# Performance work log

Hardware: AMD Instinct MI355X
Metric: run time of the kernel (lower is better)

## Reference

```python
import jax, jax.numpy as jnp
from jax import lax
import numpy as np

NUM_LABELS = 15
LABEL_TO_ID = {"O": 0, "B-PERSON": 1, "I-PERSON": 2, "B-LOCATION": 3, "I-LOCATION": 4,
               "B-ORGANIZATION": 5, "I-ORGANIZATION": 6, "B-PHONE": 7, "I-PHONE": 8,
               "B-EMAIL": 9, "I-EMAIL": 10, "B-ID_NUMBER": 11, "I-ID_NUMBER": 12,
               "B-ADDRESS": 13, "I-ADDRESS": 14}


def _pii_constraints():
    """Replicates EnhancedPIICRF._setup_transition_constraints."""
    forbidden = -10000.0
    c = np.zeros((NUM_LABELS, NUM_LABELS), dtype=np.float32)
    pii_types = ['PERSON', 'LOCATION', 'ORGANIZATION', 'PHONE', 'EMAIL', 'ID_NUMBER', 'ADDRESS']
    for t in pii_types:
        b_idx = LABEL_TO_ID[f'B-{t}']
        i_idx = LABEL_TO_ID[f'I-{t}']
        for o in pii_types:
            if o != t:
                c[LABEL_TO_ID[f'B-{o}'], i_idx] = forbidden
        if t in ['PHONE', 'EMAIL', 'ID_NUMBER']:
            c[i_idx, i_idx] = -1.0
    return jnp.asarray(c)


def setup_inputs() -> dict:
    key = jax.random.key(0)
    k1, k2, k3, k4, k5 = jax.random.split(key, 5)
    B, T, L = 512, 4096, NUM_LABELS
    emissions = jax.random.normal(k1, (B, T, L), dtype=jnp.float32)
    labels = jax.random.randint(k2, (B, T), 0, L, dtype=jnp.int64)
    mask = jnp.ones((B, T), dtype=jnp.bool_)
    # torchcrf init: uniform(-0.1, 0.1); constraints added to transitions
    transitions = jax.random.uniform(k3, (L, L), jnp.float32, -0.1, 0.1) + _pii_constraints()
    start_transitions = jax.random.uniform(k4, (L,), jnp.float32, -0.1, 0.1)
    end_transitions = jax.random.uniform(k5, (L,), jnp.float32, -0.1, 0.1)
    return {"emissions": emissions, "transitions": transitions,
            "start_transitions": start_transitions, "end_transitions": end_transitions,
            "labels": labels, "mask": mask}


def reference(emissions, transitions, start_transitions, end_transitions, labels, mask):
    """loss = -mean log-likelihood (torchcrf reduction='mean')."""
    B, T, L = emissions.shape
    maskf = mask.astype(emissions.dtype)
    labels = labels.astype(jnp.int32)

    # ---- numerator: score of the gold path (fully vectorized) ----
    em_score = jnp.take_along_axis(emissions, labels[..., None], axis=2)[..., 0]  # [B,T]
    em_score = (em_score * maskf).sum(axis=1)
    trans_score = (transitions[labels[:, :-1], labels[:, 1:]] * maskf[:, 1:]).sum(axis=1)
    seq_ends = mask.sum(axis=1).astype(jnp.int32) - 1
    last_tags = labels[jnp.arange(B), seq_ends]
    numerator = (start_transitions[labels[:, 0]] + em_score + trans_score
                 + end_transitions[last_tags])

    # ---- denominator: forward algorithm (log-sum-exp recurrence) ----
    alpha0 = start_transitions[None, :] + emissions[:, 0]  # [B,L]

    def step(alpha, xs):
        em_t, m_t = xs  # [B,L], [B]
        nxt = jax.nn.logsumexp(alpha[:, :, None] + transitions[None], axis=1) + em_t
        return jnp.where(m_t[:, None], nxt, alpha), None

    em_T = jnp.swapaxes(emissions, 0, 1)[1:]   # [T-1,B,L]
    mk_T = jnp.swapaxes(mask, 0, 1)[1:]        # [T-1,B]
    alpha, _ = lax.scan(step, alpha0, (em_T, mk_T))
    denominator = jax.nn.logsumexp(alpha + end_transitions[None, :], axis=1)

    llh = numerator - denominator
    return -jnp.mean(llh)
```

## Files before the change

### kernel.cpp

```cpp
#include <hip/hip_runtime.h>


typedef __attribute__((ext_vector_type(8))) __bf16 bf16x8;
typedef __attribute__((ext_vector_type(4))) float f32x4;
typedef __attribute__((ext_vector_type(2))) float f32x2;

#define BATCH 512
#define TLEN  4096
#define NCH   16
#define CLEN  256
#define LOG2E 1.44269504088896340736f
#define LN2   0.69314718055994530942f

__device__ __forceinline__ int pack_bf16_pair(float lo, float hi){
  return __builtin_amdgcn_perm(__float_as_uint(hi), __float_as_uint(lo), 0x07060302);
}

__global__ __launch_bounds__(256) void crf_chunk_kernel(
    const float* __restrict__ em, const float* __restrict__ trans,
    const int* __restrict__ labels,
    float* __restrict__ wsM, float* __restrict__ wsS, float* __restrict__ wsNum)
{
  const int tid   = threadIdx.x;
  const int lane  = tid & 63;
  const int col   = lane & 15;
  const int g     = lane >> 4;
  const int wid   = blockIdx.x * 4 + (tid >> 6);
  const int b     = wid >> 4;
  const int c     = wid & (NCH - 1);
  const int t0    = 1 + c * CLEN;
  const int colc  = (col < 15) ? col : 14;
  const long bT   = (long)b * TLEN;

  const float* emb = em + (bT + t0) * 15 + colc;
  float eb[8], ebn[8];

  #define LOADE(buf, rr) { const float* _p = emb + (rr) * 120; \
    _Pragma("unroll") for (int u = 0; u < 8; ++u) (buf)[u] = _p[u * 15]; }

  LOADE(eb, 0);

  {
    const int tA = c * CLEN + lane * 4;
    const int4 lv = *reinterpret_cast<const int4*>(labels + bT + tA);
    const int lpm1 = __shfl(lv.w, lane - 1);
    const float* emA = em + (bT + tA) * 15;
    float a = 0.f;
    float a0 = emA[lv.x] + trans[lpm1 * 15 + lv.x];
    if (lane > 0) a += a0;
    a += emA[15 + lv.y] + trans[lv.x * 15 + lv.y];
    a += emA[30 + lv.z] + trans[lv.y * 15 + lv.z];
    a += emA[45 + lv.w] + trans[lv.z * 15 + lv.w];
    if (lane == 63 && c < NCH - 1){
      const int te = (c + 1) * CLEN;
      const int le = labels[bT + te];
      a += em[(bT + te) * 15 + le] + trans[lv.w * 15 + le];
    }
    #pragma unroll
    for (int off = 1; off < 64; off <<= 1) a += __shfl_xor(a, off);
    if (lane == 0) wsNum[wid] = a;
  }

  f32x2 wa01, wa23;
  {
    float wv[4];
    #pragma unroll
    for (int j = 0; j < 4; ++j){
      const int row = 4 * g + j;
      wv[j] = (row < 15 && col < 15)
            ? __builtin_amdgcn_exp2f(trans[row * 15 + col] * LOG2E) : 0.f;
    }
    wa01.x = wv[0]; wa01.y = wv[1]; wa23.x = wv[2]; wa23.y = wv[3];
  }

  union { bf16x8 v; int i[4]; } af, bfr;
  af.i[2] = 0; af.i[3] = 0;
  bfr.i[2] = 0; bfr.i[3] = 0;

  f32x4 d;
  #pragma unroll
  for (int r = 0; r < 4; ++r) d[r] = (4 * g + r == col) ? 1.f : 0.f;

  const f32x4 zero4 = {0.f, 0.f, 0.f, 0.f};
  int Ki = 0;

  auto body = [&](float* ebuf, bool renorm) {
    float addend = 0.f;
    if (renorm){
      const int bits = __builtin_amdgcn_readfirstlane(__float_as_int(d[0]));
      const int K = ((bits >> 23) & 0xff) - 127;
      Ki += K;
      addend = (float)(-K);
    }
    #pragma unroll
    for (int u = 0; u < 8; ++u){
      const float x = (u == 0) ? __builtin_fmaf(ebuf[0], LOG2E, addend)
                               : ebuf[u] * LOG2E;
      const float E = __builtin_amdgcn_exp2f(x);
      const f32x2 e01 = wa01 * E, e23 = wa23 * E;
      af.i[0]  = pack_bf16_pair(e01.x, e01.y);
      af.i[1]  = pack_bf16_pair(e23.x, e23.y);
      bfr.i[0] = pack_bf16_pair(d[0], d[1]);
      bfr.i[1] = pack_bf16_pair(d[2], d[3]);
      d = __builtin_amdgcn_mfma_f32_16x16x32_bf16(af.v, bfr.v, zero4, 0, 0, 0);
    }
  };

  if (c != NCH - 1){
    #pragma unroll 1
    for (int rr = 0; rr < 16; ++rr){
      LOADE(ebn, 2 * rr + 1);
      body(eb, rr != 0);
      LOADE(eb, 2 * rr + 2);
      body(ebn, true);
    }
  } else {
    #pragma unroll 1
    for (int rr = 0; rr < 15; ++rr){
      LOADE(ebn, 2 * rr + 1);
      body(eb, rr != 0);
      LOADE(eb, 2 * rr + 2);
      body(ebn, true);
    }
    float ebt[7];
    { const float* p = emb + 31 * 120;
      #pragma unroll
      for (int u = 0; u < 7; ++u) ebt[u] = p[u * 15]; }
    body(eb, true);
    {
      const int bits = __builtin_amdgcn_readfirstlane(__float_as_int(d[0]));
      const int K = ((bits >> 23) & 0xff) - 127;
      Ki += K;
      const float addend = (float)(-K);
      #pragma unroll
      for (int u = 0; u < 7; ++u){
        const float x = (u == 0) ? __builtin_fmaf(ebt[0], LOG2E, addend)
                                 : ebt[u] * LOG2E;
        const float E = __builtin_amdgcn_exp2f(x);
        const f32x2 e01 = wa01 * E, e23 = wa23 * E;
        af.i[0]  = pack_bf16_pair(e01.x, e01.y);
        af.i[1]  = pack_bf16_pair(e23.x, e23.y);
        bfr.i[0] = pack_bf16_pair(d[0], d[1]);
        bfr.i[1] = pack_bf16_pair(d[2], d[3]);
        d = __builtin_amdgcn_mfma_f32_16x16x32_bf16(af.v, bfr.v, zero4, 0, 0, 0);
      }
    }
  }

  #undef LOADE

  *reinterpret_cast<f32x4*>(wsM + (long)wid * 256 + lane * 4) = d;
  if (lane == 0) wsS[wid] = (float)Ki;
}

__global__ __launch_bounds__(256) void crf_combine_kernel(
    const float* __restrict__ em, const float* __restrict__ startT,
    const float* __restrict__ endT, const int* __restrict__ labels,
    const float* __restrict__ wsM, const float* __restrict__ wsS,
    const float* __restrict__ wsNum, float* __restrict__ out)
{
  const int lane = threadIdx.x & 63;
  const int b = blockIdx.x * 4 + (threadIdx.x >> 6);
  const int n = lane & 15;
  const int nc = (n < 15) ? n : 0;
  const long bT = (long)b * TLEN;

  float v = (n < 15)
          ? __builtin_amdgcn_exp2f((startT[nc] + em[bT * 15 + nc]) * LOG2E) : 0.f;
  float ST = 0.f;

  float np = wsNum[b * NCH + n];
  #pragma unroll
  for (int off = 1; off < 16; off <<= 1) np += __shfl_xor(np, off);

  const int srcl = 16 * (n >> 2) + n;

  for (int c = 0; c < NCH; ++c){
    const f32x4 m4 = *reinterpret_cast<const f32x4*>(
        wsM + ((long)(b * NCH + c)) * 256 + lane * 4);
    float p0 = m4[0] * v, p1 = m4[1] * v, p2 = m4[2] * v, p3 = m4[3] * v;
    #pragma unroll
    for (int off = 1; off < 16; off <<= 1){
      p0 += __shfl_xor(p0, off); p1 += __shfl_xor(p1, off);
      p2 += __shfl_xor(p2, off); p3 += __shfl_xor(p3, off);
    }
    const float ysel = (n & 2) ? ((n & 1) ? p3 : p2) : ((n & 1) ? p1 : p0);
    v = __shfl(ysel, srcl);
    ST += wsS[b * NCH + c];
    float mx = v;
    #pragma unroll
    for (int off = 1; off < 16; off <<= 1) mx = fmaxf(mx, __shfl_xor(mx, off));
    v *= __builtin_amdgcn_rcpf(mx);
    ST += __builtin_amdgcn_logf(mx);
  }

  float w = (n < 15) ? v * __builtin_amdgcn_exp2f(endT[nc] * LOG2E) : 0.f;
  #pragma unroll
  for (int off = 1; off < 16; off <<= 1) w += __shfl_xor(w, off);

  if (lane == 0){
    const float den = (__builtin_amdgcn_logf(w) + ST) * LN2;
    const int l0 = labels[bT];
    const int lT = labels[bT + TLEN - 1];
    const float num = np + startT[l0] + em[bT * 15 + l0] + endT[lT];
    atomicAdd(out, (den - num) * (1.0f / BATCH));
  }
}

extern "C" void kernel_launch(void* const* d_in, const int* in_sizes, int n_in,
                              void* d_out, int out_size, void* d_ws, size_t ws_size,
                              hipStream_t stream)
{
  const float* em     = (const float*)d_in[0];
  const float* trans  = (const float*)d_in[1];
  const float* startT = (const float*)d_in[2];
  const float* endT   = (const float*)d_in[3];
  const int*   labels = (const int*)d_in[4];
  float* out = (float*)d_out;

  float* wsNum = (float*)d_ws;
  float* wsS   = (float*)((char*)d_ws + 32768);
  float* wsM   = (float*)((char*)d_ws + 65536);

  hipMemsetAsync(d_out, 0, sizeof(float), stream);

  crf_chunk_kernel<<<BATCH * NCH / 4, 256, 0, stream>>>(em, trans, labels, wsM, wsS, wsNum);
  crf_combine_kernel<<<BATCH / 4, 256, 0, stream>>>(em, startT, endT, labels, wsM, wsS, wsNum, out);
}
```

Measured before the change: 275.6 us.

## Interleave two independent chunk recurrences per wave and store chunk matrices as bf16

Each wave now runs two independent 128-step chunk recurrences, A and B, and alternates their exp/pack/MFMA steps. This is meant to hide the dependent MFMA latency of the serial chain. The chunk count doubles to 32 while the number of waves stays the same, and the per-chunk transfer matrices are written to the workspace in bf16 to halve that traffic. The cost is more registers per wave (launch bounds now request 8 blocks per CU) and a combine pass with twice as many serial matrix-vector steps.

```diff
diff --git a/kernel.cpp b/kernel.cpp
--- a/kernel.cpp
+++ b/kernel.cpp
@@ -7,8 +7,8 @@
 
 #define BATCH 512
 #define TLEN  4096
-#define NCH   16
-#define CLEN  256
+#define NCH   32
+#define CLEN  128
 #define LOG2E 1.44269504088896340736f
 #define LN2   0.69314718055994530942f
 
@@ -16,10 +16,10 @@
   return __builtin_amdgcn_perm(__float_as_uint(hi), __float_as_uint(lo), 0x07060302);
 }
 
-__global__ __launch_bounds__(256) void crf_chunk_kernel(
+__global__ __launch_bounds__(256, 8) void crf_chunk_kernel(
     const float* __restrict__ em, const float* __restrict__ trans,
     const int* __restrict__ labels,
-    float* __restrict__ wsM, float* __restrict__ wsS, float* __restrict__ wsNum)
+    unsigned* __restrict__ wsM, float* __restrict__ wsS, float* __restrict__ wsNum)
 {
   const int tid   = threadIdx.x;
   const int lane  = tid & 63;
@@ -27,21 +27,25 @@
   const int g     = lane >> 4;
   const int wid   = blockIdx.x * 4 + (tid >> 6);
   const int b     = wid >> 4;
-  const int c     = wid & (NCH - 1);
-  const int t0    = 1 + c * CLEN;
+  const int p     = wid & 15;
+  const int t0A   = 1 + (2 * p) * CLEN;
   const int colc  = (col < 15) ? col : 14;
   const long bT   = (long)b * TLEN;
 
-  const float* emb = em + (bT + t0) * 15 + colc;
-  float eb[8], ebn[8];
-
-  #define LOADE(buf, rr) { const float* _p = emb + (rr) * 120; \
-    _Pragma("unroll") for (int u = 0; u < 8; ++u) (buf)[u] = _p[u * 15]; }
-
-  LOADE(eb, 0);
+  const float* baseA  = em + (bT + t0A) * 15;
+  const float* baseB  = baseA + CLEN * 15;
+  const float* baseB2 = (p == 15) ? (baseB - 15) : baseB;
+
+  float ebA[8], ebAn[8], ebB[8], ebBn[8];
+
+  #define LOADE(buf, base, rr) { const float* _p = (base) + (rr) * 120; \
+    _Pragma("unroll") for (int _u = 0; _u < 8; ++_u) (buf)[_u] = _p[_u * 15 + colc]; }
+
+  LOADE(ebA, baseA, 0);
+  LOADE(ebB, baseB, 0);
 
   {
-    const int tA = c * CLEN + lane * 4;
+    const int tA = p * 256 + lane * 4;
     const int4 lv = *reinterpret_cast<const int4*>(labels + bT + tA);
     const int lpm1 = __shfl(lv.w, lane - 1);
     const float* emA = em + (bT + tA) * 15;
@@ -51,8 +55,8 @@
     a += emA[15 + lv.y] + trans[lv.x * 15 + lv.y];
     a += emA[30 + lv.z] + trans[lv.y * 15 + lv.z];
     a += emA[45 + lv.w] + trans[lv.z * 15 + lv.w];
-    if (lane == 63 && c < NCH - 1){
-      const int te = (c + 1) * CLEN;
+    if (lane == 63 && p < 15){
+      const int te = (p + 1) * 256;
       const int le = labels[bT + te];
       a += em[(bT + te) * 15 + le] + trans[lv.w * 15 + le];
     }
@@ -60,6 +64,9 @@
     for (int off = 1; off < 64; off <<= 1) a += __shfl_xor(a, off);
     if (lane == 0) wsNum[wid] = a;
   }
+
+  LOADE(ebAn, baseA, 1);
+  LOADE(ebBn, baseB, 1);
 
   f32x2 wa01, wa23;
   {
@@ -73,90 +80,98 @@
     wa01.x = wv[0]; wa01.y = wv[1]; wa23.x = wv[2]; wa23.y = wv[3];
   }
 
-  union { bf16x8 v; int i[4]; } af, bfr;
-  af.i[2] = 0; af.i[3] = 0;
-  bfr.i[2] = 0; bfr.i[3] = 0;
-
-  f32x4 d;
+  union U { bf16x8 v; int i[4]; };
+  U afA, bfrA, afB, bfrB;
+  afA.i[2] = 0; afA.i[3] = 0; bfrA.i[2] = 0; bfrA.i[3] = 0;
+  afB.i[2] = 0; afB.i[3] = 0; bfrB.i[2] = 0; bfrB.i[3] = 0;
+
+  f32x4 dA, dB;
   #pragma unroll
-  for (int r = 0; r < 4; ++r) d[r] = (4 * g + r == col) ? 1.f : 0.f;
+  for (int r = 0; r < 4; ++r){
+    dA[r] = (4 * g + r == col) ? 1.f : 0.f;
+    dB[r] = dA[r];
+  }
 
   const f32x4 zero4 = {0.f, 0.f, 0.f, 0.f};
-  int Ki = 0;
-
-  auto body = [&](float* ebuf, bool renorm) {
-    float addend = 0.f;
-    if (renorm){
-      const int bits = __builtin_amdgcn_readfirstlane(__float_as_int(d[0]));
-      const int K = ((bits >> 23) & 0xff) - 127;
-      Ki += K;
-      addend = (float)(-K);
-    }
+  int KiA = 0, KiB = 0;
+
+  #define STEP(dd, af_, bf_, E) { \
+    const f32x2 _e01 = wa01 * (E), _e23 = wa23 * (E); \
+    af_.i[0] = pack_bf16_pair(_e01.x, _e01.y); \
+    af_.i[1] = pack_bf16_pair(_e23.x, _e23.y); \
+    bf_.i[0] = pack_bf16_pair((dd)[0], (dd)[1]); \
+    bf_.i[1] = pack_bf16_pair((dd)[2], (dd)[3]); \
+    (dd) = __builtin_amdgcn_mfma_f32_16x16x32_bf16(af_.v, bf_.v, zero4, 0, 0, 0); }
+
+  auto renorm_add = [&](f32x4& dd, int& Ki) -> float {
+    const int bits = __builtin_amdgcn_readfirstlane(__float_as_int(dd[0]));
+    const int K = ((bits >> 23) & 0xff) - 127;
+    Ki += K;
+    return (float)(-K);
+  };
+
+  auto dbl = [&](float* eA, float* eB, bool renA, bool renB){
+    const float addA = renA ? renorm_add(dA, KiA) : 0.f;
+    const float addB = renB ? renorm_add(dB, KiB) : 0.f;
     #pragma unroll
     for (int u = 0; u < 8; ++u){
-      const float x = (u == 0) ? __builtin_fmaf(ebuf[0], LOG2E, addend)
-                               : ebuf[u] * LOG2E;
-      const float E = __builtin_amdgcn_exp2f(x);
-      const f32x2 e01 = wa01 * E, e23 = wa23 * E;
-      af.i[0]  = pack_bf16_pair(e01.x, e01.y);
-      af.i[1]  = pack_bf16_pair(e23.x, e23.y);
-      bfr.i[0] = pack_bf16_pair(d[0], d[1]);
-      bfr.i[1] = pack_bf16_pair(d[2], d[3]);
-      d = __builtin_amdgcn_mfma_f32_16x16x32_bf16(af.v, bfr.v, zero4, 0, 0, 0);
+      const float EA = __builtin_amdgcn_exp2f(
+          (u == 0) ? __builtin_fmaf(eA[0], LOG2E, addA) : eA[u] * LOG2E);
+      STEP(dA, afA, bfrA, EA);
+      const float EB = __builtin_amdgcn_exp2f(
+          (u == 0) ? __builtin_fmaf(eB[0], LOG2E, addB) : eB[u] * LOG2E);
+      STEP(dB, afB, bfrB, EB);
     }
   };
 
-  if (c != NCH - 1){
-    #pragma unroll 1
-    for (int rr = 0; rr < 16; ++rr){
-      LOADE(ebn, 2 * rr + 1);
-      body(eb, rr != 0);
-      LOADE(eb, 2 * rr + 2);
-      body(ebn, true);
-    }
+  #pragma unroll 1
+  for (int k = 0; k < 7; ++k){
+    dbl(ebA, ebB, k > 0, k > 0);
+    LOADE(ebA, baseA, 2 * k + 2);
+    LOADE(ebB, baseB, 2 * k + 2);
+    dbl(ebAn, ebBn, true, true);
+    LOADE(ebAn, baseA, 2 * k + 3);
+    { const float* bB = (2 * k + 3 == 15) ? baseB2 : baseB;
+      LOADE(ebBn, bB, 2 * k + 3); }
+  }
+
+  dbl(ebA, ebB, true, true);
+  if (p < 15){
+    dbl(ebAn, ebBn, true, true);
   } else {
-    #pragma unroll 1
-    for (int rr = 0; rr < 15; ++rr){
-      LOADE(ebn, 2 * rr + 1);
-      body(eb, rr != 0);
-      LOADE(eb, 2 * rr + 2);
-      body(ebn, true);
-    }
-    float ebt[7];
-    { const float* p = emb + 31 * 120;
-      #pragma unroll
-      for (int u = 0; u < 7; ++u) ebt[u] = p[u * 15]; }
-    body(eb, true);
-    {
-      const int bits = __builtin_amdgcn_readfirstlane(__float_as_int(d[0]));
-      const int K = ((bits >> 23) & 0xff) - 127;
-      Ki += K;
-      const float addend = (float)(-K);
-      #pragma unroll
-      for (int u = 0; u < 7; ++u){
-        const float x = (u == 0) ? __builtin_fmaf(ebt[0], LOG2E, addend)
-                                 : ebt[u] * LOG2E;
-        const float E = __builtin_amdgcn_exp2f(x);
-        const f32x2 e01 = wa01 * E, e23 = wa23 * E;
-        af.i[0]  = pack_bf16_pair(e01.x, e01.y);
-        af.i[1]  = pack_bf16_pair(e23.x, e23.y);
-        bfr.i[0] = pack_bf16_pair(d[0], d[1]);
-        bfr.i[1] = pack_bf16_pair(d[2], d[3]);
-        d = __builtin_amdgcn_mfma_f32_16x16x32_bf16(af.v, bfr.v, zero4, 0, 0, 0);
-      }
-    }
+    const float addA = renorm_add(dA, KiA);
+    const float addB = renorm_add(dB, KiB);
+    #pragma unroll
+    for (int u = 0; u < 7; ++u){
+      const float EA = __builtin_amdgcn_exp2f(
+          (u == 0) ? __builtin_fmaf(ebAn[0], LOG2E, addA) : ebAn[u] * LOG2E);
+      STEP(dA, afA, bfrA, EA);
+      const float EB = __builtin_amdgcn_exp2f(
+          (u == 0) ? __builtin_fmaf(ebBn[1], LOG2E, addB) : ebBn[u + 1] * LOG2E);
+      STEP(dB, afB, bfrB, EB);
+    }
+    { const float EA = __builtin_amdgcn_exp2f(ebAn[7] * LOG2E);
+      STEP(dA, afA, bfrA, EA); }
   }
 
   #undef LOADE
 
-  *reinterpret_cast<f32x4*>(wsM + (long)wid * 256 + lane * 4) = d;
-  if (lane == 0) wsS[wid] = (float)Ki;
+  const int cA = b * NCH + 2 * p;
+  {
+    uint2 sA; sA.x = (unsigned)pack_bf16_pair(dA[0], dA[1]);
+              sA.y = (unsigned)pack_bf16_pair(dA[2], dA[3]);
+    *reinterpret_cast<uint2*>(wsM + (long)cA * 128 + lane * 2) = sA;
+    uint2 sB; sB.x = (unsigned)pack_bf16_pair(dB[0], dB[1]);
+              sB.y = (unsigned)pack_bf16_pair(dB[2], dB[3]);
+    *reinterpret_cast<uint2*>(wsM + (long)(cA + 1) * 128 + lane * 2) = sB;
+  }
+  if (lane == 0){ wsS[cA] = (float)KiA; wsS[cA + 1] = (float)KiB; }
 }
 
 __global__ __launch_bounds__(256) void crf_combine_kernel(
     const float* __restrict__ em, const float* __restrict__ startT,
     const float* __restrict__ endT, const int* __restrict__ labels,
-    const float* __restrict__ wsM, const float* __restrict__ wsS,
+    const unsigned* __restrict__ wsM, const float* __restrict__ wsS,
     const float* __restrict__ wsNum, float* __restrict__ out)
 {
   const int lane = threadIdx.x & 63;
@@ -169,16 +184,20 @@
           ? __builtin_amdgcn_exp2f((startT[nc] + em[bT * 15 + nc]) * LOG2E) : 0.f;
   float ST = 0.f;
 
-  float np = wsNum[b * NCH + n];
+  float np = wsNum[b * 16 + n];
   #pragma unroll
   for (int off = 1; off < 16; off <<= 1) np += __shfl_xor(np, off);
 
   const int srcl = 16 * (n >> 2) + n;
 
   for (int c = 0; c < NCH; ++c){
-    const f32x4 m4 = *reinterpret_cast<const f32x4*>(
-        wsM + ((long)(b * NCH + c)) * 256 + lane * 4);
-    float p0 = m4[0] * v, p1 = m4[1] * v, p2 = m4[2] * v, p3 = m4[3] * v;
+    const uint2 mm = *reinterpret_cast<const uint2*>(
+        wsM + (long)(b * NCH + c) * 128 + lane * 2);
+    const float m0 = __int_as_float((int)(mm.x << 16));
+    const float m1 = __int_as_float((int)(mm.x & 0xffff0000u));
+    const float m2 = __int_as_float((int)(mm.y << 16));
+    const float m3 = __int_as_float((int)(mm.y & 0xffff0000u));
+    float p0 = m0 * v, p1 = m1 * v, p2 = m2 * v, p3 = m3 * v;
     #pragma unroll
     for (int off = 1; off < 16; off <<= 1){
       p0 += __shfl_xor(p0, off); p1 += __shfl_xor(p1, off);
@@ -218,12 +237,12 @@
   const int*   labels = (const int*)d_in[4];
   float* out = (float*)d_out;
 
-  float* wsNum = (float*)d_ws;
-  float* wsS   = (float*)((char*)d_ws + 32768);
-  float* wsM   = (float*)((char*)d_ws + 65536);
+  float*    wsNum = (float*)d_ws;
+  float*    wsS   = (float*)((char*)d_ws + 32768);
+  unsigned* wsM   = (unsigned*)((char*)d_ws + 98304);
 
   hipMemsetAsync(d_out, 0, sizeof(float), stream);
 
-  crf_chunk_kernel<<<BATCH * NCH / 4, 256, 0, stream>>>(em, trans, labels, wsM, wsS, wsNum);
+  crf_chunk_kernel<<<BATCH * 16 / 4, 256, 0, stream>>>(em, trans, labels, wsM, wsS, wsNum);
   crf_combine_kernel<<<BATCH / 4, 256, 0, stream>>>(em, startT, endT, labels, wsM, wsS, wsNum, out);
 }
```

Result: no change. 277.7 us (+0.7%).
